# Kernel tuning notes

Hardware: AMD Instinct MI355X
Metric: run time of the kernel (lower is better)

The kernel has to match this reference:

```python
import jax, jax.numpy as jnp
import numpy as np

MIN_NUMBER = -1e32


def setup_inputs() -> dict:
    key = jax.random.key(0)
    k1, k2, k3, k4, k5 = jax.random.split(key, 5)
    B, S, H, Q = 32, 2048, 2048, 1024
    rnn_out = jax.random.normal(k1, (B, S, H), dtype=jnp.float32)
    reversed_top_h_t = jax.random.normal(k2, (B, Q), dtype=jnp.float32)
    attention_mask = jnp.ones((B, S), dtype=jnp.int32)
    # parameters (scaled like default torch inits)
    Wa = jax.random.normal(k3, (Q, Q), dtype=jnp.float32) / np.sqrt(Q)
    Ua = jax.random.normal(k4, (Q, H), dtype=jnp.float32) / np.sqrt(H)   # Conv1d k=1 weight [out,in]
    Va = jax.random.normal(k5, (Q,), dtype=jnp.float32) / np.sqrt(Q)     # Conv1d q->1 weight
    return {
        "rnn_out": rnn_out,
        "reversed_top_h_t": reversed_top_h_t,
        "attention_mask": attention_mask,
        "Wa": Wa,
        "Ua": Ua,
        "Va": Va,
    }


def reference(rnn_out, reversed_top_h_t, attention_mask, Wa, Ua, Va):
    # rnn_out: [B, S, H]; reversed_top_h_t: [B, Q]; attention_mask: [B, S]
    c1 = reversed_top_h_t @ Wa.T                      # [B, Q]  (nn.Linear, no bias)
    c2 = jnp.einsum("qh,bsh->bqs", Ua, rnn_out)       # [B, Q, S] (1x1 conv over hiddens)
    c4 = jnp.tanh(c1[:, :, None] + c2)                # broadcast add + tanh
    e = jnp.einsum("q,bqs->bs", Va, c4)               # [B, S] scores (1x1 conv q->1)
    e = jnp.where(attention_mask == 0, MIN_NUMBER, e)
    a = jax.nn.softmax(e, axis=1)                     # [B, S]
    context_hidden = jnp.einsum("bsh,bs->bh", rnn_out, a)  # [B, H]
    # dropout is identity at inference (p=0)
    return context_hidden
```

## Files before the change

kernel.cpp:

```cpp
#include <hip/hip_runtime.h>
#include <hip/hip_bf16.h>

#define Bn 32
#define Sn 2048
#define Hn 2048
#define Qn 1024
#define Mn (Bn * Sn)

#define BM 128
#define BN 128
#define BK 64

typedef __attribute__((ext_vector_type(8))) short bf16x8;
typedef __attribute__((ext_vector_type(4))) float f32x4;

__device__ __forceinline__ unsigned short f2bf(float x) {
  unsigned int u = __float_as_uint(x);
  unsigned int r = (u + 0x7FFFu + ((u >> 16) & 1u)) >> 16;
  return (unsigned short)r;
}

__device__ __forceinline__ unsigned int cvtpk(float lo, float hi) {
  unsigned int r;
  asm("v_cvt_pk_bf16_f32 %0, %1, %2" : "=v"(r) : "v"(lo), "v"(hi));
  return r;
}

__device__ __forceinline__ void gload16(const void* g, void* l) {
  __builtin_amdgcn_global_load_lds(
      (const __attribute__((address_space(1))) unsigned int*)g,
      (__attribute__((address_space(3))) unsigned int*)l, 16, 0, 0);
}

__global__ void c1_kernel(const float* __restrict__ rev,
                          const float* __restrict__ Wa,
                          float* __restrict__ c1) {
  int wid = (blockIdx.x * 256 + threadIdx.x) >> 6;
  int lane = threadIdx.x & 63;
  int b = wid >> 10;
  int q = wid & (Qn - 1);
  const float* rv = rev + (size_t)b * Qn;
  const float* wr = Wa + (size_t)q * Qn;
  float acc = 0.f;
#pragma unroll
  for (int k = 0; k < Qn; k += 64) acc += rv[k + lane] * wr[k + lane];
#pragma unroll
  for (int m = 32; m > 0; m >>= 1) acc += __shfl_xor(acc, m, 64);
  if (lane == 0) c1[wid] = acc;
}

__global__ void cvt_ua_kernel(const float* __restrict__ Ua,
                              unsigned short* __restrict__ out) {
  int i = blockIdx.x * 256 + threadIdx.x;
  float4 v = ((const float4*)Ua)[i];
  typedef __attribute__((ext_vector_type(4))) unsigned short u16x4;
  u16x4 o = {f2bf(v.x), f2bf(v.y), f2bf(v.z), f2bf(v.w)};
  *(u16x4*)(out + (size_t)i * 4) = o;
}

__global__ __launch_bounds__(256) void gemm_e_kernel(
    const float* __restrict__ A, const unsigned short* __restrict__ Bmat,
    const float* __restrict__ c1, const float* __restrict__ Va,
    float* __restrict__ e) {
  __shared__ alignas(128) float As_f[BM * BK];
  __shared__ alignas(128) unsigned short Bs[BN * BK];
  __shared__ float c1s[BN];
  __shared__ float Vas[BN];

  const int t = threadIdx.x;
  const int l = t & 63;
  const int w = t >> 6;

  int bid = blockIdx.x;
  int swz = (bid & 7) * 512 + (bid >> 3);
  int panel = swz >> 3;
  int ntile = swz & 7;
  const int m0 = panel * BM;
  const int n0 = ntile * BN;
  const int bidx = panel >> 4;

  if (t < BN) {
    c1s[t] = c1[bidx * Qn + n0 + t];
    Vas[t] = Va[n0 + t];
  }

  const int lr4 = l >> 4;
  const int lr3 = l >> 3;

  const int innerA = (l & 15) * 16;
  const int keyAe = lr4 << 4;
  const int keyAo = (4 + lr4) << 4;
  const float* pAe =
      A + (size_t)(m0 + w * 32 + lr4) * Hn + ((innerA ^ keyAe) >> 2);
  const float* pAo =
      A + (size_t)(m0 + w * 32 + 4 + lr4) * Hn + ((innerA ^ keyAo) >> 2);
  const int innerB = (l & 7) * 16;
  const int keyB = lr3 << 4;
  const unsigned short* pB =
      Bmat + (size_t)(n0 + w * 32 + lr3) * Hn + ((innerB ^ keyB) >> 1);

  char* Asb = (char*)As_f;
  char* Bsb = (char*)Bs;
  char* AsW = Asb + w * 8 * 1024;
  char* BsW = Bsb + w * 4 * 1024;

  const int wm = (w >> 1) * 64;
  const int wn = (w & 1) * 64;
  const int lrow = l & 15;
  int aoff[4], boff[4];
#pragma unroll
  for (int i = 0; i < 4; i++) {
    int r = wm + i * 16 + lrow;
    aoff[i] = (r * 256 + lr4 * 32) ^ ((r & 7) << 4);
    int rb = wn + i * 16 + lrow;
    boff[i] = (rb * 128 + lr4 * 16) ^ ((rb & 7) << 4);
  }

  f32x4 acc[4][4];
#pragma unroll
  for (int i = 0; i < 4; i++)
#pragma unroll
    for (int j = 0; j < 4; j++) acc[i][j] = (f32x4){0.f, 0.f, 0.f, 0.f};

#pragma unroll 1
  for (int kb = 0; kb < Hn; kb += BK) {
    __syncthreads();
#pragma unroll
    for (int q2 = 0; q2 < 4; q2++) {
      gload16(pAe + (size_t)q2 * 8 * Hn, AsW + (2 * q2) * 1024);
      gload16(pAo + (size_t)q2 * 8 * Hn, AsW + (2 * q2 + 1) * 1024);
    }
#pragma unroll
    for (int q = 0; q < 4; q++) {
      gload16(pB + (size_t)q * 8 * Hn, BsW + q * 1024);
    }
    pAe += BK;
    pAo += BK;
    pB += BK;
    __syncthreads();

#pragma unroll
    for (int s = 0; s < 2; s++) {
      bf16x8 af[4], bfr[4];
#pragma unroll
      for (int i = 0; i < 4; i++) {
        f32x4 lo = *(const f32x4*)(Asb + (aoff[i] + s * 128));
        f32x4 hi = *(const f32x4*)(Asb + ((aoff[i] ^ 16) + s * 128));
        union { unsigned int u[4]; bf16x8 v; } tt;
        tt.u[0] = cvtpk(lo[0], lo[1]);
        tt.u[1] = cvtpk(lo[2], lo[3]);
        tt.u[2] = cvtpk(hi[0], hi[1]);
        tt.u[3] = cvtpk(hi[2], hi[3]);
        af[i] = tt.v;
      }
#pragma unroll
      for (int j = 0; j < 4; j++)
        bfr[j] = *(const bf16x8*)(Bsb + (boff[j] ^ (s * 64)));
#pragma unroll
      for (int i = 0; i < 4; i++)
#pragma unroll
        for (int j = 0; j < 4; j++)
          acc[i][j] = __builtin_amdgcn_mfma_f32_16x16x32_bf16(
              af[i], bfr[j], acc[i][j], 0, 0, 0);
    }
  }

#pragma unroll
  for (int i = 0; i < 4; i++) {
#pragma unroll
    for (int r = 0; r < 4; r++) {
      float sum = 0.f;
#pragma unroll
      for (int j = 0; j < 4; j++) {
        int ql = wn + j * 16 + lrow;
        float x = c1s[ql] + acc[i][j][r];
        float ex = __expf(2.f * x);
        float th = 1.f - 2.f / (ex + 1.f);
        sum += Vas[ql] * th;
      }
#pragma unroll
      for (int m = 8; m > 0; m >>= 1) sum += __shfl_xor(sum, m, 16);
      if (lrow == 0) {
        int row = m0 + wm + i * 16 + ((l >> 4) << 2) + r;
        atomicAdd(&e[row], sum);
      }
    }
  }
}

__global__ void softmax_kernel(const float* __restrict__ e,
                               const int* __restrict__ mask,
                               float* __restrict__ a) {
  const int b = blockIdx.x;
  const int t = threadIdx.x;
  const int lane = t & 63;
  const int w = t >> 6;
  __shared__ float red[8];
  float v[8];
  float mx = -3.0e38f;
#pragma unroll
  for (int i = 0; i < 8; i++) {
    int s = i * 256 + t;
    float x = e[(size_t)b * Sn + s];
    if (mask[(size_t)b * Sn + s] == 0) x = -1e32f;
    v[i] = x;
    mx = fmaxf(mx, x);
  }
#pragma unroll
  for (int m = 32; m > 0; m >>= 1) mx = fmaxf(mx, __shfl_xor(mx, m, 64));
  if (lane == 0) red[w] = mx;
  __syncthreads();
  mx = fmaxf(fmaxf(red[0], red[1]), fmaxf(red[2], red[3]));
  float sm = 0.f;
#pragma unroll
  for (int i = 0; i < 8; i++) {
    v[i] = __expf(v[i] - mx);
    sm += v[i];
  }
#pragma unroll
  for (int m = 32; m > 0; m >>= 1) sm += __shfl_xor(sm, m, 64);
  if (lane == 0) red[4 + w] = sm;
  __syncthreads();
  sm = red[4] + red[5] + red[6] + red[7];
  float inv = 1.f / sm;
#pragma unroll
  for (int i = 0; i < 8; i++) a[(size_t)b * Sn + i * 256 + t] = v[i] * inv;
}

__global__ void ctx_kernel(const float* __restrict__ rnn,
                           const float* __restrict__ a,
                           float* __restrict__ out) {
  const int b = blockIdx.y;
  const int sc = blockIdx.x;
  const int t = threadIdx.x;
  __shared__ float as_[256];
  as_[t] = a[(size_t)b * Sn + sc * 256 + t];
  __syncthreads();
  float a0 = 0, a1 = 0, a2 = 0, a3 = 0, a4 = 0, a5 = 0, a6 = 0, a7 = 0;
  const float* base = rnn + ((size_t)b * Sn + sc * 256) * Hn + t * 8;
  for (int s = 0; s < 256; s++) {
    float wgt = as_[s];
    float4 v0 = *(const float4*)(base + (size_t)s * Hn);
    float4 v1 = *(const float4*)(base + (size_t)s * Hn + 4);
    a0 += wgt * v0.x; a1 += wgt * v0.y; a2 += wgt * v0.z; a3 += wgt * v0.w;
    a4 += wgt * v1.x; a5 += wgt * v1.y; a6 += wgt * v1.z; a7 += wgt * v1.w;
  }
  float* o = out + (size_t)b * Hn + t * 8;
  atomicAdd(o + 0, a0); atomicAdd(o + 1, a1);
  atomicAdd(o + 2, a2); atomicAdd(o + 3, a3);
  atomicAdd(o + 4, a4); atomicAdd(o + 5, a5);
  atomicAdd(o + 6, a6); atomicAdd(o + 7, a7);
}

extern "C" void kernel_launch(void* const* d_in, const int* in_sizes, int n_in,
                              void* d_out, int out_size, void* d_ws,
                              size_t ws_size, hipStream_t stream) {
  const float* rnn = (const float*)d_in[0];
  const float* rev = (const float*)d_in[1];
  const int* mask = (const int*)d_in[2];
  const float* Wa = (const float*)d_in[3];
  const float* Ua = (const float*)d_in[4];
  const float* Va = (const float*)d_in[5];

  char* w = (char*)d_ws;
  unsigned short* Uabf = (unsigned short*)w;
  float* c1 = (float*)(w + (size_t)4 * 1024 * 1024);
  float* e = (float*)(w + (size_t)4 * 1024 * 1024 + 128 * 1024);
  float* a = (float*)(w + (size_t)4 * 1024 * 1024 + 384 * 1024);

  hipMemsetAsync(e, 0, (size_t)Mn * sizeof(float), stream);
  hipMemsetAsync(d_out, 0, (size_t)out_size * sizeof(float), stream);

  cvt_ua_kernel<<<(Qn * Hn / 4) / 256, 256, 0, stream>>>(Ua, Uabf);
  c1_kernel<<<(Bn * Qn) / 4, 256, 0, stream>>>(rev, Wa, c1);

  gemm_e_kernel<<<(Mn / BM) * (Qn / BN), 256, 0, stream>>>(rnn, Uabf, c1, Va, e);

  softmax_kernel<<<Bn, 256, 0, stream>>>(e, mask, a);

  dim3 gc(8, Bn);
  ctx_kernel<<<gc, 256, 0, stream>>>(rnn, a, (float*)d_out);
}
```

Before: 592.6 us.

## Pre-convert activations to bf16 and use pipelined 256x256 MFMA GEMM

Adds a pass converting rnn_out to bf16 in workspace. A new 512-thread GEMM kernel with 256x256 tiles then uses double-buffered direct-to-LDS loads and a phased barrier schedule with priority hints. The context kernel reads the bf16 copy, halving its traffic. This costs an extra full read and write of the activations and a large workspace, and the context sum uses reduced precision. It falls back to the old path if the workspace is too small.

```diff
diff --git a/kernel.cpp b/kernel.cpp
--- a/kernel.cpp
+++ b/kernel.cpp
@@ -7,10 +7,6 @@
 #define Qn 1024
 #define Mn (Bn * Sn)
 
-#define BM 128
-#define BN 128
-#define BK 64
-
 typedef __attribute__((ext_vector_type(8))) short bf16x8;
 typedef __attribute__((ext_vector_type(4))) float f32x4;
 
@@ -20,6 +16,10 @@
   return (unsigned short)r;
 }
 
+__device__ __forceinline__ float bf2f(short s) {
+  return __uint_as_float(((unsigned int)(unsigned short)s) << 16);
+}
+
 __device__ __forceinline__ unsigned int cvtpk(float lo, float hi) {
   unsigned int r;
   asm("v_cvt_pk_bf16_f32 %0, %1, %2" : "=v"(r) : "v"(lo), "v"(hi));
@@ -30,6 +30,23 @@
   __builtin_amdgcn_global_load_lds(
       (const __attribute__((address_space(1))) unsigned int*)g,
       (__attribute__((address_space(3))) unsigned int*)l, 16, 0, 0);
+}
+
+__global__ void cvt_rnn_kernel(const float* __restrict__ in,
+                               unsigned short* __restrict__ out) {
+  const size_t total8 = (size_t)Mn * Hn / 8;
+  size_t i = (size_t)blockIdx.x * 256 + threadIdx.x;
+  const size_t stride = (size_t)gridDim.x * 256;
+  for (; i < total8; i += stride) {
+    float4 v0 = ((const float4*)in)[i * 2];
+    float4 v1 = ((const float4*)in)[i * 2 + 1];
+    union { unsigned int u[4]; bf16x8 v; } pk;
+    pk.u[0] = cvtpk(v0.x, v0.y);
+    pk.u[1] = cvtpk(v0.z, v0.w);
+    pk.u[2] = cvtpk(v1.x, v1.y);
+    pk.u[3] = cvtpk(v1.z, v1.w);
+    *(bf16x8*)(out + i * 8) = pk.v;
+  }
 }
 
 __global__ void c1_kernel(const float* __restrict__ rev,
@@ -58,35 +75,203 @@
   *(u16x4*)(out + (size_t)i * 4) = o;
 }
 
+#define NKT 32
+
+#define STAGE_A(kt, h)                                                        \
+  do {                                                                        \
+    int d_ = (kt) & 1;                                                        \
+    gload16(aS + (size_t)((h) * 128) * Hn + (kt) * 64,                        \
+            ldsA + d_ * 32768 + (h) * 16384 + wl);                            \
+    gload16(aS + (size_t)((h) * 128 + 64) * Hn + (kt) * 64,                   \
+            ldsA + d_ * 32768 + (h) * 16384 + 8192 + wl);                     \
+  } while (0)
+
+#define STAGE_B(kt, h)                                                        \
+  do {                                                                        \
+    int d_ = (kt) & 1;                                                        \
+    gload16(bS + (size_t)((h) * 128) * Hn + (kt) * 64,                        \
+            ldsB + d_ * 32768 + (h) * 16384 + wl);                            \
+    gload16(bS + (size_t)((h) * 128 + 64) * Hn + (kt) * 64,                   \
+            ldsB + d_ * 32768 + (h) * 16384 + 8192 + wl);                     \
+  } while (0)
+
+#define VW4                                                                   \
+  do {                                                                        \
+    asm volatile("s_waitcnt vmcnt(4)");                                       \
+    __builtin_amdgcn_sched_barrier(0);                                        \
+  } while (0)
+#define VW0                                                                   \
+  do {                                                                        \
+    asm volatile("s_waitcnt vmcnt(0)");                                       \
+    __builtin_amdgcn_sched_barrier(0);                                        \
+  } while (0)
+#define NOPW ((void)0)
+
+#define PHASE(d, qm, qn, ISSUE, WAITV)                                        \
+  do {                                                                        \
+    if ((qn) == 0) {                                                          \
+      _Pragma("unroll") for (int ii = 0; ii < 4; ii++) {                      \
+        afr[ii][0] = *(const bf16x8*)(ldsA + (d) * 32768 + rA +               \
+                                      ((qm) * 64 + ii * 16) * 128 + cA0);     \
+        afr[ii][1] = *(const bf16x8*)(ldsA + (d) * 32768 + rA +               \
+                                      ((qm) * 64 + ii * 16) * 128 + cA1);     \
+      }                                                                       \
+    }                                                                         \
+    if ((qm) == 0) {                                                          \
+      _Pragma("unroll") for (int jj = 0; jj < 2; jj++) {                      \
+        bfr[(qn) * 2 + jj][0] =                                               \
+            *(const bf16x8*)(ldsB + (d) * 32768 + rB +                        \
+                             (((qn) * 2 + jj) * 16) * 128 + cA0);             \
+        bfr[(qn) * 2 + jj][1] =                                               \
+            *(const bf16x8*)(ldsB + (d) * 32768 + rB +                        \
+                             (((qn) * 2 + jj) * 16) * 128 + cA1);             \
+      }                                                                       \
+    }                                                                         \
+    ISSUE;                                                                    \
+    __builtin_amdgcn_s_barrier();                                             \
+    asm volatile("s_waitcnt lgkmcnt(0)");                                     \
+    __builtin_amdgcn_sched_barrier(0);                                        \
+    __builtin_amdgcn_s_setprio(1);                                            \
+    _Pragma("unroll") for (int ii = 0; ii < 4; ii++)                          \
+        _Pragma("unroll") for (int jj = 0; jj < 2; jj++)                      \
+            _Pragma("unroll") for (int ks = 0; ks < 2; ks++)                  \
+                acc[(qm) * 4 + ii][(qn) * 2 + jj] =                           \
+        __builtin_amdgcn_mfma_f32_16x16x32_bf16(                              \
+            afr[ii][ks], bfr[(qn) * 2 + jj][ks],                              \
+            acc[(qm) * 4 + ii][(qn) * 2 + jj], 0, 0, 0);                      \
+    __builtin_amdgcn_s_setprio(0);                                            \
+    WAITV;                                                                    \
+    __builtin_amdgcn_s_barrier();                                             \
+    __builtin_amdgcn_sched_barrier(0);                                        \
+  } while (0)
+
+__global__ __launch_bounds__(512, 2) void gemm8_kernel(
+    const unsigned short* __restrict__ A, const unsigned short* __restrict__ Bm,
+    const float* __restrict__ c1, const float* __restrict__ Va,
+    float* __restrict__ e) {
+  __shared__ __align__(128) char lds[131072];
+  __shared__ float c1s[256];
+  __shared__ float Vas[256];
+
+  const int t = threadIdx.x;
+  const int l = t & 63;
+  const int w = t >> 6;
+  const int wr = w >> 2, wc = w & 3;
+
+  int bid = blockIdx.x;
+  int swz = (bid & 7) * 128 + (bid >> 3);
+  const int mtile = swz >> 2;
+  const int ntile = swz & 3;
+  const int m0 = mtile * 256, n0 = ntile * 256;
+  const int bidx = mtile >> 3;
+
+  if (t < 256) {
+    c1s[t] = c1[bidx * Qn + n0 + t];
+    Vas[t] = Va[n0 + t];
+  }
+
+  const int sr = t >> 3;
+  const int sj = (t & 7) ^ (sr & 7);
+  const unsigned short* aS = A + (size_t)(m0 + sr) * Hn + sj * 8;
+  const unsigned short* bS = Bm + (size_t)(n0 + sr) * Hn + sj * 8;
+  char* ldsA = lds;
+  char* ldsB = lds + 65536;
+  const int wl = w * 1024;
+
+  const int xk = l & 7;
+  const int lr4 = l >> 4;
+  const int cA0 = ((0 * 4 + lr4) ^ xk) * 16;
+  const int cA1 = ((1 * 4 + lr4) ^ xk) * 16;
+  const int rA = (wr * 128 + (l & 15)) * 128;
+  const int rB = (wc * 64 + (l & 15)) * 128;
+
+  f32x4 acc[8][4];
+#pragma unroll
+  for (int i = 0; i < 8; i++)
+#pragma unroll
+    for (int j = 0; j < 4; j++) acc[i][j] = (f32x4){0.f, 0.f, 0.f, 0.f};
+
+  bf16x8 afr[4][2], bfr[4][2];
+
+  asm volatile("s_waitcnt vmcnt(0)");
+  __builtin_amdgcn_sched_barrier(0);
+  STAGE_A(0, 0);
+  STAGE_A(0, 1);
+  STAGE_B(0, 0);
+  STAGE_B(0, 1);
+  STAGE_B(1, 0);
+  STAGE_B(1, 1);
+  asm volatile("s_waitcnt vmcnt(4)");
+  __builtin_amdgcn_sched_barrier(0);
+  __builtin_amdgcn_s_barrier();
+  __builtin_amdgcn_sched_barrier(0);
+
+#pragma unroll 1
+  for (int it = 0; it < NKT / 2; ++it) {
+    const int ko = 2 * it + 1;
+    const int k2 = 2 * it + 2, k3 = 2 * it + 3;
+    const bool nx = (it < NKT / 2 - 1);
+    PHASE(0, 0, 0, STAGE_A(ko, 0), NOPW);
+    PHASE(0, 0, 1, STAGE_A(ko, 1), NOPW);
+    PHASE(0, 1, 0, if (nx) STAGE_B(k2, 0), NOPW);
+    PHASE(0, 1, 1, if (nx) STAGE_B(k2, 1), if (nx) VW4; else VW0);
+    PHASE(1, 0, 0, if (nx) STAGE_A(k2, 0), NOPW);
+    PHASE(1, 0, 1, if (nx) STAGE_A(k2, 1), NOPW);
+    PHASE(1, 1, 0, if (nx) STAGE_B(k3, 0), NOPW);
+    PHASE(1, 1, 1, if (nx) STAGE_B(k3, 1), if (nx) VW4; else VW0);
+  }
+
+#pragma unroll
+  for (int i = 0; i < 8; i++) {
+#pragma unroll
+    for (int r = 0; r < 4; r++) {
+      float sum = 0.f;
+#pragma unroll
+      for (int j = 0; j < 4; j++) {
+        int ql = wc * 64 + j * 16 + (l & 15);
+        float x = c1s[ql] + acc[i][j][r];
+        float ex = __expf(2.f * x);
+        sum += Vas[ql] * (1.f - 2.f / (ex + 1.f));
+      }
+#pragma unroll
+      for (int m = 8; m > 0; m >>= 1) sum += __shfl_xor(sum, m, 16);
+      if ((l & 15) == 0) {
+        int row = m0 + wr * 128 + i * 16 + (l >> 4) * 4 + r;
+        atomicAdd(&e[row], sum);
+      }
+    }
+  }
+}
+
+#define BMf 128
+#define BNf 128
+#define BKf 64
 __global__ __launch_bounds__(256) void gemm_e_kernel(
     const float* __restrict__ A, const unsigned short* __restrict__ Bmat,
     const float* __restrict__ c1, const float* __restrict__ Va,
     float* __restrict__ e) {
-  __shared__ alignas(128) float As_f[BM * BK];
-  __shared__ alignas(128) unsigned short Bs[BN * BK];
-  __shared__ float c1s[BN];
-  __shared__ float Vas[BN];
+  __shared__ alignas(128) float As_f[BMf * BKf];
+  __shared__ alignas(128) unsigned short Bs[BNf * BKf];
+  __shared__ float c1s[BNf];
+  __shared__ float Vas[BNf];
 
   const int t = threadIdx.x;
   const int l = t & 63;
   const int w = t >> 6;
-
   int bid = blockIdx.x;
   int swz = (bid & 7) * 512 + (bid >> 3);
   int panel = swz >> 3;
   int ntile = swz & 7;
-  const int m0 = panel * BM;
-  const int n0 = ntile * BN;
+  const int m0 = panel * BMf;
+  const int n0 = ntile * BNf;
   const int bidx = panel >> 4;
 
-  if (t < BN) {
+  if (t < BNf) {
     c1s[t] = c1[bidx * Qn + n0 + t];
     Vas[t] = Va[n0 + t];
   }
-
   const int lr4 = l >> 4;
   const int lr3 = l >> 3;
-
   const int innerA = (l & 15) * 16;
   const int keyAe = lr4 << 4;
   const int keyAo = (4 + lr4) << 4;
@@ -123,7 +308,7 @@
     for (int j = 0; j < 4; j++) acc[i][j] = (f32x4){0.f, 0.f, 0.f, 0.f};
 
 #pragma unroll 1
-  for (int kb = 0; kb < Hn; kb += BK) {
+  for (int kb = 0; kb < Hn; kb += BKf) {
     __syncthreads();
 #pragma unroll
     for (int q2 = 0; q2 < 4; q2++) {
@@ -131,17 +316,15 @@
       gload16(pAo + (size_t)q2 * 8 * Hn, AsW + (2 * q2 + 1) * 1024);
     }
 #pragma unroll
-    for (int q = 0; q < 4; q++) {
-      gload16(pB + (size_t)q * 8 * Hn, BsW + q * 1024);
-    }
-    pAe += BK;
-    pAo += BK;
-    pB += BK;
+    for (int q = 0; q < 4; q++) gload16(pB + (size_t)q * 8 * Hn, BsW + q * 1024);
+    pAe += BKf;
+    pAo += BKf;
+    pB += BKf;
     __syncthreads();
 
 #pragma unroll
     for (int s = 0; s < 2; s++) {
-      bf16x8 af[4], bfr[4];
+      bf16x8 af[4], bfv[4];
 #pragma unroll
       for (int i = 0; i < 4; i++) {
         f32x4 lo = *(const f32x4*)(Asb + (aoff[i] + s * 128));
@@ -155,13 +338,13 @@
       }
 #pragma unroll
       for (int j = 0; j < 4; j++)
-        bfr[j] = *(const bf16x8*)(Bsb + (boff[j] ^ (s * 64)));
+        bfv[j] = *(const bf16x8*)(Bsb + (boff[j] ^ (s * 64)));
 #pragma unroll
       for (int i = 0; i < 4; i++)
 #pragma unroll
         for (int j = 0; j < 4; j++)
           acc[i][j] = __builtin_amdgcn_mfma_f32_16x16x32_bf16(
-              af[i], bfr[j], acc[i][j], 0, 0, 0);
+              af[i], bfv[j], acc[i][j], 0, 0, 0);
     }
   }
 
@@ -175,8 +358,7 @@
         int ql = wn + j * 16 + lrow;
         float x = c1s[ql] + acc[i][j][r];
         float ex = __expf(2.f * x);
-        float th = 1.f - 2.f / (ex + 1.f);
-        sum += Vas[ql] * th;
+        sum += Vas[ql] * (1.f - 2.f / (ex + 1.f));
       }
 #pragma unroll
       for (int m = 8; m > 0; m >>= 1) sum += __shfl_xor(sum, m, 16);
@@ -225,6 +407,29 @@
   float inv = 1.f / sm;
 #pragma unroll
   for (int i = 0; i < 8; i++) a[(size_t)b * Sn + i * 256 + t] = v[i] * inv;
+}
+
+__global__ void ctx_bf16_kernel(const unsigned short* __restrict__ rnnbf,
+                                const float* __restrict__ a,
+                                float* __restrict__ out) {
+  const int b = blockIdx.y;
+  const int sc = blockIdx.x;
+  const int t = threadIdx.x;
+  __shared__ float as_[256];
+  as_[t] = a[(size_t)b * Sn + sc * 256 + t];
+  __syncthreads();
+  float ac[8] = {0, 0, 0, 0, 0, 0, 0, 0};
+  const unsigned short* base =
+      rnnbf + ((size_t)b * Sn + sc * 256) * Hn + t * 8;
+  for (int s = 0; s < 256; s++) {
+    float wgt = as_[s];
+    bf16x8 v = *(const bf16x8*)(base + (size_t)s * Hn);
+#pragma unroll
+    for (int k = 0; k < 8; k++) ac[k] += wgt * bf2f(v[k]);
+  }
+  float* o = out + (size_t)b * Hn + t * 8;
+#pragma unroll
+  for (int k = 0; k < 8; k++) atomicAdd(o + k, ac[k]);
 }
 
 __global__ void ctx_kernel(const float* __restrict__ rnn,
@@ -262,22 +467,44 @@
   const float* Ua = (const float*)d_in[4];
   const float* Va = (const float*)d_in[5];
 
+  const size_t RNBF = (size_t)Mn * Hn * 2;
+  const size_t NEED = RNBF + 4194304 + 131072 + 262144 + 262144;
+
   char* w = (char*)d_ws;
-  unsigned short* Uabf = (unsigned short*)w;
-  float* c1 = (float*)(w + (size_t)4 * 1024 * 1024);
-  float* e = (float*)(w + (size_t)4 * 1024 * 1024 + 128 * 1024);
-  float* a = (float*)(w + (size_t)4 * 1024 * 1024 + 384 * 1024);
-
-  hipMemsetAsync(e, 0, (size_t)Mn * sizeof(float), stream);
-  hipMemsetAsync(d_out, 0, (size_t)out_size * sizeof(float), stream);
-
-  cvt_ua_kernel<<<(Qn * Hn / 4) / 256, 256, 0, stream>>>(Ua, Uabf);
-  c1_kernel<<<(Bn * Qn) / 4, 256, 0, stream>>>(rev, Wa, c1);
-
-  gemm_e_kernel<<<(Mn / BM) * (Qn / BN), 256, 0, stream>>>(rnn, Uabf, c1, Va, e);
-
-  softmax_kernel<<<Bn, 256, 0, stream>>>(e, mask, a);
-
-  dim3 gc(8, Bn);
-  ctx_kernel<<<gc, 256, 0, stream>>>(rnn, a, (float*)d_out);
-}
+  if (ws_size >= NEED) {
+    unsigned short* rnnbf = (unsigned short*)w;
+    unsigned short* Uabf = (unsigned short*)(w + RNBF);
+    float* c1 = (float*)(w + RNBF + 4194304);
+    float* e = (float*)(w + RNBF + 4194304 + 131072);
+    float* a = (float*)(w + RNBF + 4194304 + 131072 + 262144);
+
+    hipMemsetAsync(e, 0, (size_t)Mn * sizeof(float), stream);
+    hipMemsetAsync(d_out, 0, (size_t)out_size * sizeof(float), stream);
+
+    cvt_rnn_kernel<<<4096, 256, 0, stream>>>(rnn, rnnbf);
+    cvt_ua_kernel<<<(Qn * Hn / 4) / 256, 256, 0, stream>>>(Ua, Uabf);
+    c1_kernel<<<(Bn * Qn) / 4, 256, 0, stream>>>(rev, Wa, c1);
+
+    gemm8_kernel<<<(Mn / 256) * (Qn / 256), 512, 0, stream>>>(rnnbf, Uabf, c1,
+                                                              Va, e);
+    softmax_kernel<<<Bn, 256, 0, stream>>>(e, mask, a);
+    dim3 gc(8, Bn);
+    ctx_bf16_kernel<<<gc, 256, 0, stream>>>(rnnbf, a, (float*)d_out);
+  } else {
+    unsigned short* Uabf = (unsigned short*)w;
+    float* c1 = (float*)(w + (size_t)4 * 1024 * 1024);
+    float* e = (float*)(w + (size_t)4 * 1024 * 1024 + 128 * 1024);
+    float* a = (float*)(w + (size_t)4 * 1024 * 1024 + 384 * 1024);
+
+    hipMemsetAsync(e, 0, (size_t)Mn * sizeof(float), stream);
+    hipMemsetAsync(d_out, 0, (size_t)out_size * sizeof(float), stream);
+
+    cvt_ua_kernel<<<(Qn * Hn / 4) / 256, 256, 0, stream>>>(Ua, Uabf);
+    c1_kernel<<<(Bn * Qn) / 4, 256, 0, stream>>>(rev, Wa, c1);
+    gemm_e_kernel<<<(Mn / BMf) * (Qn / BNf), 256, 0, stream>>>(rnn, Uabf, c1,
+                                                               Va, e);
+    softmax_kernel<<<Bn, 256, 0, stream>>>(e, mask, a);
+    dim3 gc(8, Bn);
+    ctx_kernel<<<gc, 256, 0, stream>>>(rnn, a, (float*)d_out);
+  }
+}
```

New measurement: 500.7 us. 15.5% less time.

## Rewrite score GEMM as 256x256 8-wave double-buffered pipeline with bf16 A staging

Applied to the files above, without the earlier changes.

Replaces the 128x128, 4-wave GEMM with a 256x256 tile computed by 8 waves. A is loaded from global into registers, converted to bf16 once, and written to double-buffered LDS, while B is staged with direct global-to-LDS loads. The K loop is split into phases that interleave MFMA work with the next tile's loads, using explicit vmcnt waits, barriers and setprio. The goal is more operand reuse per tile, conversion done once per element instead of on every LDS read, and overlap of memory traffic with matrix math. In exchange it uses much more LDS and registers per block, which limits occupancy, and the hand-written wait counts are fragile.

```diff
diff --git a/kernel.cpp b/kernel.cpp
--- a/kernel.cpp
+++ b/kernel.cpp
@@ -6,10 +6,6 @@
 #define Hn 2048
 #define Qn 1024
 #define Mn (Bn * Sn)
-
-#define BM 128
-#define BN 128
-#define BK 64
 
 typedef __attribute__((ext_vector_type(8))) short bf16x8;
 typedef __attribute__((ext_vector_type(4))) float f32x4;
@@ -58,130 +54,189 @@
   *(u16x4*)(out + (size_t)i * 4) = o;
 }
 
-__global__ __launch_bounds__(256) void gemm_e_kernel(
-    const float* __restrict__ A, const unsigned short* __restrict__ Bmat,
+#define NKT 32
+
+#define VMW(n)                                                                \
+  do {                                                                        \
+    asm volatile("s_waitcnt vmcnt(" #n ")");                                  \
+    __builtin_amdgcn_sched_barrier(0);                                        \
+  } while (0)
+#define NOPW ((void)0)
+
+#define STAGE_B(kt, h)                                                        \
+  do {                                                                        \
+    int d_ = (kt) & 1;                                                        \
+    gload16(bS + (size_t)((h) * 128) * Hn + (kt) * 64,                        \
+            ldsB + d_ * 32768 + (h) * 16384 + wl);                            \
+    gload16(bS + (size_t)((h) * 128 + 64) * Hn + (kt) * 64,                   \
+            ldsB + d_ * 32768 + (h) * 16384 + 8192 + wl);                     \
+  } while (0)
+
+#define ALOAD(kt, h, V)                                                       \
+  do {                                                                        \
+    V[0] = *(const float4*)(aF + (size_t)((h) * 128) * Hn + (kt) * 64);       \
+    V[1] = *(const float4*)(aF + (size_t)((h) * 128) * Hn + (kt) * 64 + 4);   \
+    V[2] = *(const float4*)(aF + (size_t)((h) * 128 + 64) * Hn + (kt) * 64);  \
+    V[3] = *(const float4*)(aF + (size_t)((h) * 128 + 64) * Hn + (kt) * 64 +  \
+                            4);                                               \
+  } while (0)
+
+#define AWRITE(kt, h, V)                                                      \
+  do {                                                                        \
+    int d_ = (kt) & 1;                                                        \
+    union { unsigned int u[4]; bf16x8 v; } p0_, p1_;                          \
+    p0_.u[0] = cvtpk(V[0].x, V[0].y); p0_.u[1] = cvtpk(V[0].z, V[0].w);       \
+    p0_.u[2] = cvtpk(V[1].x, V[1].y); p0_.u[3] = cvtpk(V[1].z, V[1].w);       \
+    p1_.u[0] = cvtpk(V[2].x, V[2].y); p1_.u[1] = cvtpk(V[2].z, V[2].w);       \
+    p1_.u[2] = cvtpk(V[3].x, V[3].y); p1_.u[3] = cvtpk(V[3].z, V[3].w);       \
+    *(bf16x8*)(ldsA + d_ * 32768 + (h) * 16384 + t * 16) = p0_.v;             \
+    *(bf16x8*)(ldsA + d_ * 32768 + (h) * 16384 + 8192 + t * 16) = p1_.v;      \
+  } while (0)
+
+#define PHASE(d, qm, qn, ISSUE, WAITV)                                        \
+  do {                                                                        \
+    if ((qn) == 0) {                                                          \
+      _Pragma("unroll") for (int ii = 0; ii < 4; ii++) {                      \
+        afr[ii][0] = *(const bf16x8*)(ldsA + (d) * 32768 + rA +               \
+                                      ((qm) * 64 + ii * 16) * 128 + cA0);     \
+        afr[ii][1] = *(const bf16x8*)(ldsA + (d) * 32768 + rA +               \
+                                      ((qm) * 64 + ii * 16) * 128 + cA1);     \
+      }                                                                       \
+    }                                                                         \
+    if ((qm) == 0) {                                                          \
+      _Pragma("unroll") for (int jj = 0; jj < 2; jj++) {                      \
+        bfr[(qn) * 2 + jj][0] =                                               \
+            *(const bf16x8*)(ldsB + (d) * 32768 + rB +                        \
+                             (((qn) * 2 + jj) * 16) * 128 + cA0);             \
+        bfr[(qn) * 2 + jj][1] =                                               \
+            *(const bf16x8*)(ldsB + (d) * 32768 + rB +                        \
+                             (((qn) * 2 + jj) * 16) * 128 + cA1);             \
+      }                                                                       \
+    }                                                                         \
+    ISSUE;                                                                    \
+    __builtin_amdgcn_s_barrier();                                             \
+    asm volatile("s_waitcnt lgkmcnt(0)");                                     \
+    __builtin_amdgcn_sched_barrier(0);                                        \
+    __builtin_amdgcn_s_setprio(1);                                            \
+    _Pragma("unroll") for (int ii = 0; ii < 4; ii++)                          \
+        _Pragma("unroll") for (int jj = 0; jj < 2; jj++)                      \
+            _Pragma("unroll") for (int ks = 0; ks < 2; ks++)                  \
+                acc[(qm) * 4 + ii][(qn) * 2 + jj] =                           \
+        __builtin_amdgcn_mfma_f32_16x16x32_bf16(                              \
+            afr[ii][ks], bfr[(qn) * 2 + jj][ks],                              \
+            acc[(qm) * 4 + ii][(qn) * 2 + jj], 0, 0, 0);                      \
+    __builtin_amdgcn_s_setprio(0);                                            \
+    WAITV;                                                                    \
+    __builtin_amdgcn_s_barrier();                                             \
+    __builtin_amdgcn_sched_barrier(0);                                        \
+  } while (0)
+
+__global__ __launch_bounds__(512, 2) void gemm8_kernel(
+    const float* __restrict__ A, const unsigned short* __restrict__ Bm,
     const float* __restrict__ c1, const float* __restrict__ Va,
     float* __restrict__ e) {
-  __shared__ alignas(128) float As_f[BM * BK];
-  __shared__ alignas(128) unsigned short Bs[BN * BK];
-  __shared__ float c1s[BN];
-  __shared__ float Vas[BN];
+  __shared__ __align__(128) char lds[131072];
+  __shared__ float c1s[256];
+  __shared__ float Vas[256];
 
   const int t = threadIdx.x;
   const int l = t & 63;
   const int w = t >> 6;
+  const int wr = w >> 2, wc = w & 3;
 
   int bid = blockIdx.x;
-  int swz = (bid & 7) * 512 + (bid >> 3);
-  int panel = swz >> 3;
-  int ntile = swz & 7;
-  const int m0 = panel * BM;
-  const int n0 = ntile * BN;
-  const int bidx = panel >> 4;
-
-  if (t < BN) {
+  int swz = (bid & 7) * 128 + (bid >> 3);
+  const int mtile = swz >> 2;
+  const int ntile = swz & 3;
+  const int m0 = mtile * 256, n0 = ntile * 256;
+  const int bidx = mtile >> 3;
+
+  const int sr = t >> 3;
+  const int sj = (t & 7) ^ (sr & 7);
+  const float* aF = A + (size_t)(m0 + sr) * Hn + sj * 8;
+  const unsigned short* bS = Bm + (size_t)(n0 + sr) * Hn + sj * 8;
+  char* ldsA = lds;
+  char* ldsB = lds + 65536;
+  const int wl = w * 1024;
+
+  const int xk = l & 7;
+  const int lr4 = l >> 4;
+  const int cA0 = ((0 * 4 + lr4) ^ xk) * 16;
+  const int cA1 = ((1 * 4 + lr4) ^ xk) * 16;
+  const int rA = (wr * 128 + (l & 15)) * 128;
+  const int rB = (wc * 64 + (l & 15)) * 128;
+
+  f32x4 acc[8][4];
+#pragma unroll
+  for (int i = 0; i < 8; i++)
+#pragma unroll
+    for (int j = 0; j < 4; j++) acc[i][j] = (f32x4){0.f, 0.f, 0.f, 0.f};
+
+  bf16x8 afr[4][2], bfr[4][2];
+  float4 sE0[4], sE1[4], sO0[4], sO1[4];
+
+  ALOAD(0, 0, sE0);
+  ALOAD(0, 1, sE1);
+  STAGE_B(0, 0);
+  STAGE_B(0, 1);
+  ALOAD(1, 0, sO0);
+  ALOAD(1, 1, sO1);
+  STAGE_B(1, 0);
+  STAGE_B(1, 1);
+  VMW(16);
+  AWRITE(0, 0, sE0);
+  AWRITE(0, 1, sE1);
+  VMW(12);
+  asm volatile("s_waitcnt lgkmcnt(0)");
+  __builtin_amdgcn_sched_barrier(0);
+  __builtin_amdgcn_s_barrier();
+  __builtin_amdgcn_sched_barrier(0);
+
+#pragma unroll 1
+  for (int it = 0; it < NKT / 2; ++it) {
+    const int ko = 2 * it + 1;
+    const int k2 = 2 * it + 2, k3 = 2 * it + 3;
+    const bool nx = (it < NKT / 2 - 1);
+    PHASE(0, 0, 0,
+          { VMW(8); AWRITE(ko, 0, sO0); if (nx) ALOAD(k2, 0, sE0); }, NOPW);
+    PHASE(0, 0, 1,
+          { if (nx) { VMW(8); } else { VMW(4); }
+            AWRITE(ko, 1, sO1);
+            if (nx) ALOAD(k2, 1, sE1); }, NOPW);
+    PHASE(0, 1, 0, { if (nx) STAGE_B(k2, 0); }, NOPW);
+    PHASE(0, 1, 1, { if (nx) STAGE_B(k2, 1); },
+          { if (nx) { VMW(12); } else { VMW(0); } });
+    PHASE(1, 0, 0,
+          { if (nx) { VMW(8); AWRITE(k2, 0, sE0); ALOAD(k3, 0, sO0); } }, NOPW);
+    PHASE(1, 0, 1,
+          { if (nx) { VMW(8); AWRITE(k2, 1, sE1); ALOAD(k3, 1, sO1); } }, NOPW);
+    PHASE(1, 1, 0, { if (nx) STAGE_B(k3, 0); }, NOPW);
+    PHASE(1, 1, 1, { if (nx) STAGE_B(k3, 1); },
+          { if (nx) { VMW(12); } });
+  }
+
+  if (t < 256) {
     c1s[t] = c1[bidx * Qn + n0 + t];
     Vas[t] = Va[n0 + t];
   }
-
-  const int lr4 = l >> 4;
-  const int lr3 = l >> 3;
-
-  const int innerA = (l & 15) * 16;
-  const int keyAe = lr4 << 4;
-  const int keyAo = (4 + lr4) << 4;
-  const float* pAe =
-      A + (size_t)(m0 + w * 32 + lr4) * Hn + ((innerA ^ keyAe) >> 2);
-  const float* pAo =
-      A + (size_t)(m0 + w * 32 + 4 + lr4) * Hn + ((innerA ^ keyAo) >> 2);
-  const int innerB = (l & 7) * 16;
-  const int keyB = lr3 << 4;
-  const unsigned short* pB =
-      Bmat + (size_t)(n0 + w * 32 + lr3) * Hn + ((innerB ^ keyB) >> 1);
-
-  char* Asb = (char*)As_f;
-  char* Bsb = (char*)Bs;
-  char* AsW = Asb + w * 8 * 1024;
-  char* BsW = Bsb + w * 4 * 1024;
-
-  const int wm = (w >> 1) * 64;
-  const int wn = (w & 1) * 64;
-  const int lrow = l & 15;
-  int aoff[4], boff[4];
-#pragma unroll
-  for (int i = 0; i < 4; i++) {
-    int r = wm + i * 16 + lrow;
-    aoff[i] = (r * 256 + lr4 * 32) ^ ((r & 7) << 4);
-    int rb = wn + i * 16 + lrow;
-    boff[i] = (rb * 128 + lr4 * 16) ^ ((rb & 7) << 4);
-  }
-
-  f32x4 acc[4][4];
-#pragma unroll
-  for (int i = 0; i < 4; i++)
-#pragma unroll
-    for (int j = 0; j < 4; j++) acc[i][j] = (f32x4){0.f, 0.f, 0.f, 0.f};
-
-#pragma unroll 1
-  for (int kb = 0; kb < Hn; kb += BK) {
-    __syncthreads();
-#pragma unroll
-    for (int q2 = 0; q2 < 4; q2++) {
-      gload16(pAe + (size_t)q2 * 8 * Hn, AsW + (2 * q2) * 1024);
-      gload16(pAo + (size_t)q2 * 8 * Hn, AsW + (2 * q2 + 1) * 1024);
-    }
-#pragma unroll
-    for (int q = 0; q < 4; q++) {
-      gload16(pB + (size_t)q * 8 * Hn, BsW + q * 1024);
-    }
-    pAe += BK;
-    pAo += BK;
-    pB += BK;
-    __syncthreads();
-
-#pragma unroll
-    for (int s = 0; s < 2; s++) {
-      bf16x8 af[4], bfr[4];
-#pragma unroll
-      for (int i = 0; i < 4; i++) {
-        f32x4 lo = *(const f32x4*)(Asb + (aoff[i] + s * 128));
-        f32x4 hi = *(const f32x4*)(Asb + ((aoff[i] ^ 16) + s * 128));
-        union { unsigned int u[4]; bf16x8 v; } tt;
-        tt.u[0] = cvtpk(lo[0], lo[1]);
-        tt.u[1] = cvtpk(lo[2], lo[3]);
-        tt.u[2] = cvtpk(hi[0], hi[1]);
-        tt.u[3] = cvtpk(hi[2], hi[3]);
-        af[i] = tt.v;
-      }
-#pragma unroll
-      for (int j = 0; j < 4; j++)
-        bfr[j] = *(const bf16x8*)(Bsb + (boff[j] ^ (s * 64)));
-#pragma unroll
-      for (int i = 0; i < 4; i++)
-#pragma unroll
-        for (int j = 0; j < 4; j++)
-          acc[i][j] = __builtin_amdgcn_mfma_f32_16x16x32_bf16(
-              af[i], bfr[j], acc[i][j], 0, 0, 0);
-    }
-  }
-
-#pragma unroll
-  for (int i = 0; i < 4; i++) {
+  __syncthreads();
+
+#pragma unroll
+  for (int i = 0; i < 8; i++) {
 #pragma unroll
     for (int r = 0; r < 4; r++) {
       float sum = 0.f;
 #pragma unroll
       for (int j = 0; j < 4; j++) {
-        int ql = wn + j * 16 + lrow;
+        int ql = wc * 64 + j * 16 + (l & 15);
         float x = c1s[ql] + acc[i][j][r];
         float ex = __expf(2.f * x);
-        float th = 1.f - 2.f / (ex + 1.f);
-        sum += Vas[ql] * th;
+        sum += Vas[ql] * (1.f - 2.f / (ex + 1.f));
       }
 #pragma unroll
       for (int m = 8; m > 0; m >>= 1) sum += __shfl_xor(sum, m, 16);
-      if (lrow == 0) {
-        int row = m0 + wm + i * 16 + ((l >> 4) << 2) + r;
+      if ((l & 15) == 0) {
+        int row = m0 + wr * 128 + i * 16 + (l >> 4) * 4 + r;
         atomicAdd(&e[row], sum);
       }
     }
@@ -264,9 +319,9 @@
 
   char* w = (char*)d_ws;
   unsigned short* Uabf = (unsigned short*)w;
-  float* c1 = (float*)(w + (size_t)4 * 1024 * 1024);
-  float* e = (float*)(w + (size_t)4 * 1024 * 1024 + 128 * 1024);
-  float* a = (float*)(w + (size_t)4 * 1024 * 1024 + 384 * 1024);
+  float* c1 = (float*)(w + 4194304);
+  float* e = (float*)(w + 4194304 + 131072);
+  float* a = (float*)(w + 4194304 + 131072 + 262144);
 
   hipMemsetAsync(e, 0, (size_t)Mn * sizeof(float), stream);
   hipMemsetAsync(d_out, 0, (size_t)out_size * sizeof(float), stream);
@@ -274,8 +329,8 @@
   cvt_ua_kernel<<<(Qn * Hn / 4) / 256, 256, 0, stream>>>(Ua, Uabf);
   c1_kernel<<<(Bn * Qn) / 4, 256, 0, stream>>>(rev, Wa, c1);
 
-  gemm_e_kernel<<<(Mn / BM) * (Qn / BN), 256, 0, stream>>>(rnn, Uabf, c1, Va, e);
-
+  gemm8_kernel<<<(Mn / 256) * (Qn / 256), 512, 0, stream>>>(rnn, Uabf, c1, Va,
+                                                            e);
   softmax_kernel<<<Bn, 256, 0, stream>>>(e, mask, a);
 
   dim3 gc(8, Bn);
```

Result: slower. 947.0 us (+59.8%).
